# Performance work log

Measured on AMD Instinct MI355X. Metric: run time of the kernel, lower is better.

## Reference

```python
import jax, jax.numpy as jnp
import numpy as np

TOP_K = 30
NUM_RBF = 16
MAX_REL = 32  # max_relative_feature
EDGE_FEATURES = 128
NUM_PE = 16
EDGE_IN = NUM_PE + NUM_RBF * 25  # 416

B, L = 8, 1024


def setup_inputs() -> dict:
    key = jax.random.key(0)
    ks = jax.random.split(key, 8)
    X = jax.random.normal(ks[0], (B, L, 4, 3), dtype=jnp.float32)
    mask = jnp.ones((B, L), dtype=jnp.float32)
    residue_idx = jnp.arange(B * L, dtype=jnp.int64 if jax.config.jax_enable_x64 else jnp.int32).reshape(B, L) % L
    chain_labels = jnp.sort(jax.random.randint(ks[1], (B, L), 0, 4), axis=-1)
    # learned params
    W_pe = jax.random.normal(ks[2], (NUM_PE, 2 * MAX_REL + 2), dtype=jnp.float32) * 0.05
    b_pe = jnp.zeros((NUM_PE,), dtype=jnp.float32)
    W_edge = jax.random.normal(ks[3], (EDGE_FEATURES, EDGE_IN), dtype=jnp.float32) * 0.05
    ln_w = jnp.ones((EDGE_FEATURES,), dtype=jnp.float32)
    ln_b = jnp.zeros((EDGE_FEATURES,), dtype=jnp.float32)
    return {"X": X, "mask": mask, "residue_idx": residue_idx, "chain_labels": chain_labels,
            "W_pe": W_pe, "b_pe": b_pe, "W_edge": W_edge, "ln_w": ln_w, "ln_b": ln_b}


def reference(X, mask, residue_idx, chain_labels, W_pe, b_pe, W_edge, ln_w, ln_b):
    Bn, Ln = mask.shape
    # virtual C-beta from ideal geometry
    b = X[:, :, 1] - X[:, :, 0]
    c = X[:, :, 2] - X[:, :, 1]
    a = jnp.cross(b, c)
    Cb = -0.58273431 * a + 0.56802827 * b - 0.54067466 * c + X[:, :, 1]
    X5 = jnp.concatenate([X, Cb[:, :, None, :]], axis=2)  # [B,L,5,3]

    # kNN on CA-CA distances
    Ca = X5[:, :, 1]  # [B,L,3]
    m2 = mask[:, None, :] * mask[:, :, None]
    dX = Ca[:, None, :, :] - Ca[:, :, None, :]
    D = m2 * jnp.sqrt(jnp.sum(dX * dX, -1) + 1e-6)  # [B,L,L]
    D_max = jnp.max(D, -1, keepdims=True)
    D_adjust = D + (1.0 - m2) * D_max
    k = min(TOP_K, Ln)
    neg_vals, E_idx = jax.lax.top_k(-D_adjust, k)  # smallest-k

    # gather neighbor coords once: [B,L,K,5,3]
    batch = jnp.arange(Bn)[:, None, None]
    Xn = X5[batch, E_idx]
    # all 25 atom-pair distances to neighbors, fused: [B,L,K,5,5]
    diff = X5[:, :, None, :, None, :] - Xn[:, :, :, None, :, :]
    D_ab = jnp.sqrt(jnp.sum(diff * diff, -1) + 1e-6)
    # RBF featurization
    mu = jnp.linspace(2.0, 22.0, NUM_RBF)
    sigma = (22.0 - 2.0) / NUM_RBF
    RBF = jnp.exp(-(((D_ab[..., None] - mu) / sigma) ** 2))  # [B,L,K,5,5,16]
    # loop order in torch is c1-major, c2-minor, rbf innermost -> plain reshape matches
    RBF_all = RBF.reshape(Bn, Ln, k, 5 * 5 * NUM_RBF)

    # positional encodings
    offset = residue_idx[:, :, None] - residue_idx[:, None, :]
    offset_n = jnp.take_along_axis(offset, E_idx, axis=2)  # [B,L,K]
    d_chains = (chain_labels[:, :, None] == chain_labels[:, None, :]).astype(jnp.int32)
    E_chains = jnp.take_along_axis(d_chains, E_idx, axis=2)
    d = jnp.clip(offset_n + MAX_REL, 0, 2 * MAX_REL) * E_chains + (1 - E_chains) * (2 * MAX_REL + 1)
    d_onehot = jax.nn.one_hot(d, 2 * MAX_REL + 2, dtype=W_pe.dtype)
    E_pos = d_onehot @ W_pe.T + b_pe  # [B,L,K,16]

    E = jnp.concatenate([E_pos, RBF_all], axis=-1)  # [B,L,K,416]
    E = E @ W_edge.T  # edge_embedding, no bias
    # LayerNorm (eps=1e-5)
    mu_e = jnp.mean(E, -1, keepdims=True)
    var_e = jnp.var(E, -1, keepdims=True)
    E = (E - mu_e) / jnp.sqrt(var_e + 1e-5) * ln_w + ln_b
    return E, E_idx, X
```

## Files before the change

kernel.cpp:

```cpp
#include <hip/hip_runtime.h>
#include <math.h>

#define B_   8
#define L_   1024
#define K_   30
#define EF_  128
#define EIN_ 416
#define MAXREL_ 32

using f32x4 = __attribute__((ext_vector_type(4))) float;



__device__ __forceinline__ unsigned long long shflx64(unsigned long long v, int m)
{
    int lo = __shfl_xor((int)(unsigned)(v & 0xffffffffull), m, 64);
    int hi = __shfl_xor((int)(unsigned)(v >> 32), m, 64);
    return ((unsigned long long)(unsigned)hi << 32) | (unsigned)lo;
}
__device__ __forceinline__ unsigned long long bcast64(unsigned long long v, int srcLane)
{
    int lo = __shfl((int)(unsigned)(v & 0xffffffffull), srcLane, 64);
    int hi = __shfl((int)(unsigned)(v >> 32), srcLane, 64);
    return ((unsigned long long)(unsigned)hi << 32) | (unsigned)lo;
}

template<int NR>
__device__ __forceinline__ void bitonic_sort(unsigned long long v[NR], int lane)
{
    constexpr int E = NR * 64;
    #pragma unroll
    for (int k = 2; k <= E; k <<= 1) {
        #pragma unroll
        for (int d = k >> 1; d >= 1; d >>= 1) {
            if (d >= 64) {
                const int s = d >> 6;
                #pragma unroll
                for (int r = 0; r < NR; r++) {
                    if ((r & s) == 0) {
                        const int r2 = r | s;
                        const bool up = (((r * 64) & k) == 0);
                        unsigned long long a = v[r], b = v[r2];
                        bool al = a < b;
                        unsigned long long mn = al ? a : b, mx = al ? b : a;
                        v[r]  = up ? mn : mx;
                        v[r2] = up ? mx : mn;
                    }
                }
            } else {
                #pragma unroll
                for (int r = 0; r < NR; r++) {
                    unsigned long long pv = shflx64(v[r], d);
                    bool up    = (((r * 64 + lane) & k) == 0);
                    bool lower = ((lane & d) == 0);
                    bool keepmin = (up == lower);
                    bool mine = (v[r] < pv);
                    v[r] = (keepmin == mine) ? v[r] : pv;
                }
            }
        }
    }
}

__global__ __launch_bounds__(256) void pf_pre_topk(
    const float* __restrict__ X, const float* __restrict__ W_pe,
    const float* __restrict__ b_pe, const float* __restrict__ W_edge,
    float* __restrict__ x5p, float* __restrict__ tpe, short* __restrict__ wt8s,
    float* __restrict__ outX, float* __restrict__ outEidxF)
{
    __shared__ float ca[L_ * 3];
    __shared__ unsigned long long surv[4][128];

    int t = threadIdx.x;

    if (blockIdx.x >= 2048) {
        int id = (blockIdx.x - 2048) * 256 + t;

        if (id < B_ * L_ * 12) outX[id] = X[id];

        int id1 = id - B_ * L_ * 12;
        if (id1 >= 0 && id1 < B_ * L_) {
            const float* xp = X + (size_t)id1 * 12;
            float n0 = xp[0], n1 = xp[1], n2 = xp[2];
            float ca0 = xp[3], ca1 = xp[4], ca2 = xp[5];
            float c0 = xp[6], c1 = xp[7], c2 = xp[8];
            float o0 = xp[9], o1 = xp[10], o2 = xp[11];
            float bv0 = ca0 - n0, bv1 = ca1 - n1, bv2 = ca2 - n2;
            float cv0 = c0 - ca0, cv1 = c1 - ca1, cv2 = c2 - ca2;
            float av0 = bv1 * cv2 - bv2 * cv1;
            float av1 = bv2 * cv0 - bv0 * cv2;
            float av2 = bv0 * cv1 - bv1 * cv0;
            float cb0 = -0.58273431f * av0 + 0.56802827f * bv0 - 0.54067466f * cv0 + ca0;
            float cb1 = -0.58273431f * av1 + 0.56802827f * bv1 - 0.54067466f * cv1 + ca1;
            float cb2 = -0.58273431f * av2 + 0.56802827f * bv2 - 0.54067466f * cv2 + ca2;
            float* o = x5p + (size_t)id1 * 16;
            o[0] = n0;  o[1] = n1;  o[2] = n2;
            o[3] = ca0; o[4] = ca1; o[5] = ca2;
            o[6] = c0;  o[7] = c1;  o[8] = c2;
            o[9] = o0;  o[10] = o1; o[11] = o2;
            o[12] = cb0; o[13] = cb1; o[14] = cb2; o[15] = 0.f;
        }

        int id2 = id1 - B_ * L_;
        if (id2 >= 0 && id2 < 66 * 128) {
            int dcol = id2 >> 7, f = id2 & 127;
            const float* wrow = W_edge + (size_t)f * EIN_;
            float s = 0.f;
            #pragma unroll
            for (int p = 0; p < 16; p++) s += wrow[p] * W_pe[p * 66 + dcol];
            float sb = 0.f;
            #pragma unroll
            for (int p = 0; p < 16; p++) sb += wrow[p] * b_pe[p];
            tpe[id2] = (s + sb) * 8.0f;
        }

        int id3 = id2 - 66 * 128;
        if (id3 >= 0 && id3 < 128 * 208) {
            int f = id3 / 208, kp = (id3 - f * 208) * 2;
            float w0 = W_edge[(size_t)f * EIN_ + 16 + kp] * 8.0f;
            float w1 = W_edge[(size_t)f * EIN_ + 16 + kp + 1] * 8.0f;
            int pk = __builtin_amdgcn_cvt_pk_fp8_f32(w0, w1, 0, false);
            wt8s[f * 208 + (kp >> 1)] = (short)pk;
        }
        return;
    }

    int blk = blockIdx.x;
    int b = blk >> 8;
    const float* xb = X + (size_t)b * L_ * 12;

    for (int j = t; j < L_; j += 256) {
        ca[j * 3 + 0] = xb[j * 12 + 3];
        ca[j * 3 + 1] = xb[j * 12 + 4];
        ca[j * 3 + 2] = xb[j * 12 + 5];
    }
    __syncthreads();

    int w = t >> 6, lane = t & 63;
    int row = blk * 4 + w;
    int i = row & 1023;
    float cx = ca[i * 3 + 0], cy = ca[i * 3 + 1], cz = ca[i * 3 + 2];

    unsigned long long keys[16];
    #pragma unroll
    for (int q = 0; q < 16; q++) {
        int j = lane + 64 * q;
        float dx = ca[j * 3 + 0] - cx;
        float dy = ca[j * 3 + 1] - cy;
        float dz = ca[j * 3 + 2] - cz;
        float s = __fadd_rn(__fadd_rn(__fadd_rn(__fmul_rn(dx, dx), __fmul_rn(dy, dy)),
                                      __fmul_rn(dz, dz)), 1e-6f);
        float d = sqrtf(s);
        unsigned db = __builtin_bit_cast(unsigned, d);
        keys[q] = ((unsigned long long)db << 10) | (unsigned)j;
    }

    unsigned long long tr[8];
    #pragma unroll
    for (int q = 0; q < 8; q++)
        tr[q] = keys[q] < keys[q + 8] ? keys[q] : keys[q + 8];
    #pragma unroll
    for (int st = 4; st >= 1; st >>= 1)
        #pragma unroll
        for (int q = 0; q < st; q++)
            tr[q] = tr[q] < tr[q + st] ? tr[q] : tr[q + st];

    unsigned long long hs[1] = { tr[0] };
    bitonic_sort<1>(hs, lane);
    unsigned long long T = bcast64(hs[0], 29);

    int cnt = 0;
    #pragma unroll
    for (int q = 0; q < 16; q++) cnt += (keys[q] <= T) ? 1 : 0;
    int pre = cnt;
    #pragma unroll
    for (int off = 1; off < 64; off <<= 1) {
        int n = __shfl_up(pre, (unsigned)off, 64);
        if (lane >= off) pre += n;
    }
    int C = __shfl(pre, 63, 64);
    int base = pre - cnt;

    if (C <= 128) {
        unsigned long long* sv = surv[w];
        sv[lane] = ~0ull;
        sv[lane + 64] = ~0ull;
        int o = base;
        #pragma unroll
        for (int q = 0; q < 16; q++) {
            if (keys[q] <= T) { sv[o] = keys[q]; o++; }
        }
        __asm__ volatile("s_waitcnt lgkmcnt(0)" ::: "memory");
        unsigned long long v2[2];
        v2[0] = sv[lane];
        v2[1] = sv[lane + 64];
        bitonic_sort<2>(v2, lane);
        if (lane < K_)
            outEidxF[(size_t)row * K_ + lane] = (float)(unsigned)(v2[0] & 1023ull);
    } else {
        #pragma unroll 1
        for (int it = 0; it < K_; it++) {
            unsigned long long m = keys[0];
            #pragma unroll
            for (int q = 1; q < 16; q++) m = keys[q] < m ? keys[q] : m;
            #pragma unroll
            for (int off = 1; off < 64; off <<= 1) {
                unsigned long long o2 = shflx64(m, off);
                m = o2 < m ? o2 : m;
            }
            if (lane == 0)
                outEidxF[(size_t)row * K_ + it] = (float)(unsigned)(m & 1023ull);
            #pragma unroll
            for (int q = 0; q < 16; q++)
                keys[q] = (keys[q] == m) ? ~0ull : keys[q];
        }
    }
}

__global__ __launch_bounds__(256, 4) void pf_edge(
    const float* __restrict__ x5p, const float* __restrict__ tpe,
    const unsigned char* __restrict__ wt8, const float* __restrict__ eidxF,
    const int* __restrict__ ridx, const int* __restrict__ chain,
    const float* __restrict__ ln_w, const float* __restrict__ ln_b,
    float* __restrict__ outE)
{
    __shared__ __align__(16) unsigned char featA8[64 * 424];
    __shared__ __align__(16) float xbuf[960];
    __shared__ __align__(16) float x5c[32];
    __shared__ int dpe_s[64];

    int t = threadIdx.x;
    int lane = t & 63, w = t >> 6;
    int q = lane >> 4, m15 = lane & 15;
    int row0 = blockIdx.x * 2;
    int b = row0 >> 10;

    long breg0[13], breg1[13];
    {
        const long* wr0 = (const long*)(wt8 + (size_t)(w * 32 + m15) * 416);
        const long* wr1 = (const long*)(wt8 + (size_t)(w * 32 + 16 + m15) * 416);
        #pragma unroll
        for (int kk = 0; kk < 13; kk++) {
            breg0[kk] = wr0[kk * 4 + q];
            breg1[kk] = wr1[kk * 4 + q];
        }
    }

    if (t < 60) {
        int r = t >= 30, e = t - r * 30;
        int rowg = row0 + r;
        int j = (int)eidxF[(size_t)rowg * K_ + e];
        int off = ridx[rowg] - ridx[b * L_ + j];
        int same = (chain[rowg] == chain[b * L_ + j]);
        int dv = off + MAXREL_;
        dv = dv < 0 ? 0 : (dv > 2 * MAXREL_ ? 2 * MAXREL_ : dv);
        dpe_s[t + (r ? 2 : 0)] = same ? dv : (2 * MAXREL_ + 1);
    }
    if (t >= 60 && t < 64) {
        int p = t - 60;
        dpe_s[p < 2 ? 30 + p : 60 + p] = 0;
    }
    if (t < 240) {
        int e = t >> 2, c = t & 3;
        int r = e >= 30, ee = e - r * 30;
        int rowg = row0 + r;
        int j = (int)eidxF[(size_t)rowg * K_ + ee];
        ((float4*)xbuf)[e * 4 + c] = ((const float4*)x5p)[(size_t)(b * L_ + j) * 4 + c];
    } else if (t < 248) {
        int c = t - 240;
        ((float4*)x5c)[c] = ((const float4*)x5p)[(size_t)(row0 + (c >> 2)) * 4 + (c & 3)];
    }
    {
        int m = t >> 2, c = t & 3;
        *(int*)&featA8[m * 424 + 400 + c * 4] = 0;
    }
    __syncthreads();

    f32x4 acc[4][2];
    #pragma unroll
    for (int mt = 0; mt < 4; mt++)
        #pragma unroll
        for (int nt = 0; nt < 2; nt++)
            #pragma unroll
            for (int r = 0; r < 4; r++) {
                int m = mt * 16 + q * 4 + r;
                int f = w * 32 + nt * 16 + m15;
                acc[mt][nt][r] = tpe[dpe_s[m] * 128 + f];
            }

    for (int task = t; task < 60 * 25; task += 256) {
        int e = task / 25, p = task - e * 25;
        int A = p / 5, Bv = p - A * 5;
        int rr = (e >= 30);
        float dx = x5c[rr * 16 + A * 3 + 0] - xbuf[e * 16 + Bv * 3 + 0];
        float dy = x5c[rr * 16 + A * 3 + 1] - xbuf[e * 16 + Bv * 3 + 1];
        float dz = x5c[rr * 16 + A * 3 + 2] - xbuf[e * 16 + Bv * 3 + 2];
        float d = sqrtf(dx * dx + dy * dy + dz * dz + 1e-6f);
        d = fminf(d, 25.0f);
        float t8v = 0.8f * d - 10.1333333f;
        float t7v = t8v + 1.0666667f;
        float base8 = __expf(-t8v * t8v);
        float u     = __expf(2.1333333f * t8v);
        float base7 = __expf(-t7v * t7v);
        float uinv  = __builtin_amdgcn_rcpf(u);
        float wdn   = uinv * 0.10273980f;
        float vv[16];
        vv[8] = base8;
        float pp = base8;
        pp *= u;   vv[9]  = pp * 0.32053053f;
        pp *= u;   vv[10] = pp * 0.010555467f;
        pp *= u;   vv[11] = pp * 3.571282e-5f;
        pp *= u;   vv[12] = pp * 1.2413945e-8f;
        pp *= u;   vv[13] = pp * 4.4333619e-13f;
        pp *= u;   vv[14] = pp * 1.6266628e-18f;
        pp *= u;   vv[15] = pp * 6.1319565e-25f;
        vv[7] = base7;
        float qq = base7;
        qq *= wdn; vv[6]  = qq * 0.32053053f;
        qq *= wdn; vv[5]  = qq * 0.010555467f;
        qq *= wdn; vv[4]  = qq * 3.571282e-5f;
        qq *= wdn; vv[3]  = qq * 1.2413945e-8f;
        qq *= wdn; vv[2]  = qq * 4.4333619e-13f;
        qq *= wdn; vv[1]  = qq * 1.6266628e-18f;
        qq *= wdn; vv[0]  = qq * 6.1319565e-25f;
        int slot = e + (rr ? 2 : 0);
        int p0 = __builtin_amdgcn_cvt_pk_fp8_f32(vv[0], vv[1], 0, false);
        p0     = __builtin_amdgcn_cvt_pk_fp8_f32(vv[2], vv[3], p0, true);
        int p1 = __builtin_amdgcn_cvt_pk_fp8_f32(vv[4], vv[5], 0, false);
        p1     = __builtin_amdgcn_cvt_pk_fp8_f32(vv[6], vv[7], p1, true);
        int p2 = __builtin_amdgcn_cvt_pk_fp8_f32(vv[8], vv[9], 0, false);
        p2     = __builtin_amdgcn_cvt_pk_fp8_f32(vv[10], vv[11], p2, true);
        int p3 = __builtin_amdgcn_cvt_pk_fp8_f32(vv[12], vv[13], 0, false);
        p3     = __builtin_amdgcn_cvt_pk_fp8_f32(vv[14], vv[15], p3, true);
        long lo = (unsigned)p0 | ((long)(unsigned)p1 << 32);
        long hi = (unsigned)p2 | ((long)(unsigned)p3 << 32);
        *(long*)&featA8[slot * 424 + p * 16] = lo;
        *(long*)&featA8[slot * 424 + p * 16 + 8] = hi;
    }
    __syncthreads();

    #pragma unroll
    for (int kk = 0; kk < 13; kk++) {
        int k0 = kk * 32;
        long afr[4];
        #pragma unroll
        for (int mt = 0; mt < 4; mt++)
            afr[mt] = *(const long*)&featA8[(mt * 16 + m15) * 424 + k0 + q * 8];
        #pragma unroll
        for (int mt = 0; mt < 4; mt++) {
            acc[mt][0] = __builtin_amdgcn_mfma_f32_16x16x32_fp8_fp8(
                afr[mt], breg0[kk], acc[mt][0], 0, 0, 0);
            acc[mt][1] = __builtin_amdgcn_mfma_f32_16x16x32_fp8_fp8(
                afr[mt], breg1[kk], acc[mt][1], 0, 0, 0);
        }
    }

    float2* part = (float2*)xbuf;
    #pragma unroll
    for (int mt = 0; mt < 4; mt++)
        #pragma unroll
        for (int r = 0; r < 4; r++) {
            int m = mt * 16 + q * 4 + r;
            float sv = acc[mt][0][r] + acc[mt][1][r];
            float qv = acc[mt][0][r] * acc[mt][0][r] + acc[mt][1][r] * acc[mt][1][r];
            #pragma unroll
            for (int off = 1; off < 16; off <<= 1) {
                sv += __shfl_xor(sv, (unsigned)off, 16);
                qv += __shfl_xor(qv, (unsigned)off, 16);
            }
            if (m15 == 0) part[m * 4 + w] = make_float2(sv, qv);
        }
    __syncthreads();

    float2* muinv = (float2*)(xbuf + 512);
    if (t < 64) {
        float s = 0.f, s2 = 0.f;
        #pragma unroll
        for (int c = 0; c < 4; c++) {
            float2 pc = part[t * 4 + c];
            s += pc.x; s2 += pc.y;
        }
        float mu = s * (1.0f / 128.0f);
        float var = s2 * (1.0f / 128.0f) - mu * mu;
        var = var < 0.f ? 0.f : var;
        muinv[t] = make_float2(mu, rsqrtf(var + 6.4e-4f));
    }
    __syncthreads();

    float lw0 = ln_w[w * 32 + m15],      lb0 = ln_b[w * 32 + m15];
    float lw1 = ln_w[w * 32 + 16 + m15], lb1 = ln_b[w * 32 + 16 + m15];
    #pragma unroll
    for (int mt = 0; mt < 4; mt++)
        #pragma unroll
        for (int r = 0; r < 4; r++) {
            int m = mt * 16 + q * 4 + r;
            if ((m & 31) < 30) {
                float2 mi = muinv[m];
                float a0 = mi.y * lw0, c0 = lb0 - mi.x * a0;
                float a1 = mi.y * lw1, c1 = lb1 - mi.x * a1;
                int rowg = row0 + (m >> 5);
                int eidx = m & 31;
                size_t base = ((size_t)rowg * K_ + eidx) * 128;
                outE[base + w * 32 + m15]      = acc[mt][0][r] * a0 + c0;
                outE[base + w * 32 + 16 + m15] = acc[mt][1][r] * a1 + c1;
            }
        }
}

extern "C" void kernel_launch(void* const* d_in, const int* in_sizes, int n_in,
                              void* d_out, int out_size, void* d_ws, size_t ws_size,
                              hipStream_t stream)
{
    const float* X      = (const float*)d_in[0];
    const int*   ridx   = (const int*)d_in[2];
    const int*   chain  = (const int*)d_in[3];
    const float* W_pe   = (const float*)d_in[4];
    const float* b_pe   = (const float*)d_in[5];
    const float* W_edge = (const float*)d_in[6];
    const float* ln_w   = (const float*)d_in[7];
    const float* ln_b   = (const float*)d_in[8];

    float* outE    = (float*)d_out;
    float* outEidx = outE + (size_t)B_ * L_ * K_ * EF_;
    float* outX    = outEidx + (size_t)B_ * L_ * K_;

    float* x5p  = (float*)d_ws;
    float* tpe  = x5p + B_ * L_ * 16;
    short* wt8s = (short*)(tpe + 66 * 128);

    pf_pre_topk<<<2601, 256, 0, stream>>>(X, W_pe, b_pe, W_edge, x5p, tpe, wt8s,
                                          outX, outEidx);
    pf_edge<<<B_ * L_ / 2, 256, 0, stream>>>(x5p, tpe, (const unsigned char*)wt8s,
                                             outEidx, ridx, chain, ln_w, ln_b, outE);
}
```

Baseline: 212.8 us.

## Transpose MFMA operands for vector stores and stream weights instead of register-caching

Swaps the MFMA operand roles so the FP8 weights are the A operand and the edge features are B. Each lane then holds four consecutive output features of one edge. This allows float4 loads of the positional-encoding table init, float4 LayerNorm parameter loads and float4 output stores, and cuts the per-row shuffle reduction to two cross-quad shuffles. The 26 per-thread weight registers preloaded before the GEMM are dropped. Weight fragments are now loaded from global memory inside a non-unrolled k-loop, and launch bounds are raised to 5 blocks per CU to trade register pressure for occupancy, at the cost of repeated cached weight reads on the critical path.

```diff
diff --git a/kernel.cpp b/kernel.cpp
--- a/kernel.cpp
+++ b/kernel.cpp
@@ -217,7 +217,7 @@
     }
 }
 
-__global__ __launch_bounds__(256, 4) void pf_edge(
+__global__ __launch_bounds__(256, 5) void pf_edge(
     const float* __restrict__ x5p, const float* __restrict__ tpe,
     const unsigned char* __restrict__ wt8, const float* __restrict__ eidxF,
     const int* __restrict__ ridx, const int* __restrict__ chain,
@@ -234,17 +234,6 @@
     int q = lane >> 4, m15 = lane & 15;
     int row0 = blockIdx.x * 2;
     int b = row0 >> 10;
-
-    long breg0[13], breg1[13];
-    {
-        const long* wr0 = (const long*)(wt8 + (size_t)(w * 32 + m15) * 416);
-        const long* wr1 = (const long*)(wt8 + (size_t)(w * 32 + 16 + m15) * 416);
-        #pragma unroll
-        for (int kk = 0; kk < 13; kk++) {
-            breg0[kk] = wr0[kk * 4 + q];
-            breg1[kk] = wr1[kk * 4 + q];
-        }
-    }
 
     if (t < 60) {
         int r = t >= 30, e = t - r * 30;
@@ -278,15 +267,16 @@
 
     f32x4 acc[4][2];
     #pragma unroll
-    for (int mt = 0; mt < 4; mt++)
-        #pragma unroll
-        for (int nt = 0; nt < 2; nt++)
-            #pragma unroll
-            for (int r = 0; r < 4; r++) {
-                int m = mt * 16 + q * 4 + r;
-                int f = w * 32 + nt * 16 + m15;
-                acc[mt][nt][r] = tpe[dpe_s[m] * 128 + f];
-            }
+    for (int et = 0; et < 4; et++) {
+        int m = et * 16 + m15;
+        const float4* trow = (const float4*)(tpe + dpe_s[m] * 128);
+        #pragma unroll
+        for (int ft = 0; ft < 2; ft++) {
+            float4 v = trow[w * 8 + ft * 4 + q];
+            acc[et][ft][0] = v.x; acc[et][ft][1] = v.y;
+            acc[et][ft][2] = v.z; acc[et][ft][3] = v.w;
+        }
+    }
 
     for (int task = t; task < 60 * 25; task += 256) {
         int e = task / 25, p = task - e * 25;
@@ -339,37 +329,40 @@
     }
     __syncthreads();
 
-    #pragma unroll
-    for (int kk = 0; kk < 13; kk++) {
-        int k0 = kk * 32;
-        long afr[4];
-        #pragma unroll
-        for (int mt = 0; mt < 4; mt++)
-            afr[mt] = *(const long*)&featA8[(mt * 16 + m15) * 424 + k0 + q * 8];
-        #pragma unroll
-        for (int mt = 0; mt < 4; mt++) {
-            acc[mt][0] = __builtin_amdgcn_mfma_f32_16x16x32_fp8_fp8(
-                afr[mt], breg0[kk], acc[mt][0], 0, 0, 0);
-            acc[mt][1] = __builtin_amdgcn_mfma_f32_16x16x32_fp8_fp8(
-                afr[mt], breg1[kk], acc[mt][1], 0, 0, 0);
-        }
+    for (int k0 = 0; k0 < 416; k0 += 32) {
+        long ffr[4];
+        #pragma unroll
+        for (int et = 0; et < 4; et++)
+            ffr[et] = *(const long*)&featA8[(et * 16 + m15) * 424 + k0 + q * 8];
+        long wfr[2];
+        #pragma unroll
+        for (int ft = 0; ft < 2; ft++)
+            wfr[ft] = *(const long*)&wt8[(size_t)(w * 32 + ft * 16 + m15) * 416 + k0 + q * 8];
+        #pragma unroll
+        for (int et = 0; et < 4; et++)
+            #pragma unroll
+            for (int ft = 0; ft < 2; ft++)
+                acc[et][ft] = __builtin_amdgcn_mfma_f32_16x16x32_fp8_fp8(
+                    wfr[ft], ffr[et], acc[et][ft], 0, 0, 0);
     }
 
     float2* part = (float2*)xbuf;
     #pragma unroll
-    for (int mt = 0; mt < 4; mt++)
-        #pragma unroll
-        for (int r = 0; r < 4; r++) {
-            int m = mt * 16 + q * 4 + r;
-            float sv = acc[mt][0][r] + acc[mt][1][r];
-            float qv = acc[mt][0][r] * acc[mt][0][r] + acc[mt][1][r] * acc[mt][1][r];
-            #pragma unroll
-            for (int off = 1; off < 16; off <<= 1) {
-                sv += __shfl_xor(sv, (unsigned)off, 16);
-                qv += __shfl_xor(qv, (unsigned)off, 16);
+    for (int et = 0; et < 4; et++) {
+        float sv = 0.f, qv = 0.f;
+        #pragma unroll
+        for (int ft = 0; ft < 2; ft++)
+            #pragma unroll
+            for (int r = 0; r < 4; r++) {
+                float v = acc[et][ft][r];
+                sv += v; qv += v * v;
             }
-            if (m15 == 0) part[m * 4 + w] = make_float2(sv, qv);
-        }
+        sv += __shfl_xor(sv, 16u, 64);
+        qv += __shfl_xor(qv, 16u, 64);
+        sv += __shfl_xor(sv, 32u, 64);
+        qv += __shfl_xor(qv, 32u, 64);
+        if (q == 0) part[(et * 16 + m15) * 4 + w] = make_float2(sv, qv);
+    }
     __syncthreads();
 
     float2* muinv = (float2*)(xbuf + 512);
@@ -387,24 +380,33 @@
     }
     __syncthreads();
 
-    float lw0 = ln_w[w * 32 + m15],      lb0 = ln_b[w * 32 + m15];
-    float lw1 = ln_w[w * 32 + 16 + m15], lb1 = ln_b[w * 32 + 16 + m15];
-    #pragma unroll
-    for (int mt = 0; mt < 4; mt++)
-        #pragma unroll
-        for (int r = 0; r < 4; r++) {
-            int m = mt * 16 + q * 4 + r;
-            if ((m & 31) < 30) {
-                float2 mi = muinv[m];
-                float a0 = mi.y * lw0, c0 = lb0 - mi.x * a0;
-                float a1 = mi.y * lw1, c1 = lb1 - mi.x * a1;
-                int rowg = row0 + (m >> 5);
-                int eidx = m & 31;
-                size_t base = ((size_t)rowg * K_ + eidx) * 128;
-                outE[base + w * 32 + m15]      = acc[mt][0][r] * a0 + c0;
-                outE[base + w * 32 + 16 + m15] = acc[mt][1][r] * a1 + c1;
+    float4 lwv[2], lbv[2];
+    #pragma unroll
+    for (int ft = 0; ft < 2; ft++) {
+        lwv[ft] = ((const float4*)ln_w)[w * 8 + ft * 4 + q];
+        lbv[ft] = ((const float4*)ln_b)[w * 8 + ft * 4 + q];
+    }
+    #pragma unroll
+    for (int et = 0; et < 4; et++) {
+        int m = et * 16 + m15;
+        if ((m & 31) < 30) {
+            float2 mi = muinv[m];
+            int rowg = row0 + (m >> 5);
+            int eidx = m & 31;
+            float* dst = outE + ((size_t)rowg * K_ + eidx) * 128 + w * 32 + q * 4;
+            #pragma unroll
+            for (int ft = 0; ft < 2; ft++) {
+                float ax = mi.y * lwv[ft].x, ay = mi.y * lwv[ft].y;
+                float az = mi.y * lwv[ft].z, aw = mi.y * lwv[ft].w;
+                float4 o;
+                o.x = acc[et][ft][0] * ax + (lbv[ft].x - mi.x * ax);
+                o.y = acc[et][ft][1] * ay + (lbv[ft].y - mi.x * ay);
+                o.z = acc[et][ft][2] * az + (lbv[ft].z - mi.x * az);
+                o.w = acc[et][ft][3] * aw + (lbv[ft].w - mi.x * aw);
+                *(float4*)(dst + ft * 16) = o;
             }
         }
+    }
 }
 
 extern "C" void kernel_launch(void* const* d_in, const int* in_sizes, int n_in,
```

New measurement: 202.3 us. 4.9% less time.
